# Kernel optimization log

Hardware: AMD Instinct MI355X
Metric: run time of the kernel (lower is better)

## Reference

```python
import jax, jax.numpy as jnp
import numpy as np

B, S, H, DH = 2, 2048, 16, 64
D = H * DH  # 1024
NEG = 1e11

def setup_inputs() -> dict:
    key = jax.random.key(0)
    ks = jax.random.split(key, 4)
    std = 0.02
    return {
        "x": jax.random.normal(ks[0], (B, S, D), dtype=jnp.float32),
        "Wq": jax.random.normal(ks[1], (D, D), dtype=jnp.float32) * std,
        "bq": jnp.zeros((D,), dtype=jnp.float32),
        "Wk": jax.random.normal(ks[2], (D, D), dtype=jnp.float32) * std,
        "bk": jnp.zeros((D,), dtype=jnp.float32),
        "Wv": jax.random.normal(ks[3], (D, D), dtype=jnp.float32) * std,
        "bv": jnp.zeros((D,), dtype=jnp.float32),
    }

def reference(x, Wq, bq, Wk, bk, Wv, bv):
    # QKV projections: [B,S,D]
    q = x @ Wq + bq
    k = x @ Wk + bk
    v = x @ Wv + bv
    # split heads -> [B,H,S,DH]
    def split(t):
        return t.reshape(B, S, H, DH).transpose(0, 2, 1, 3)
    q, k, v = split(q), split(k), split(v)
    # scaled scores [B,H,S,S]
    scores = jnp.einsum("bhqd,bhkd->bhqk", q, k) / jnp.sqrt(jnp.float32(DH))
    # causal mask: query i attends to keys j <= i; original does s*m - (1-m)*1e11
    m = (jnp.arange(S)[:, None] >= jnp.arange(S)[None, :]).astype(scores.dtype)
    scores = scores * m - (1.0 - m) * NEG
    probs = jax.nn.softmax(scores, axis=-1)
    out = jnp.einsum("bhqk,bhkd->bhqd", probs, v)  # [B,H,S,DH]
    return out.transpose(0, 2, 1, 3).reshape(B, S, D)
```

## Files before the change

### kernel.cpp

```cpp
#include <hip/hip_runtime.h>
#include <hip/hip_bf16.h>
#include <stdint.h>

#define B_    2
#define S_    2048
#define H_    16
#define DH_   64
#define D_    1024
#define ND3   3072
#define MTOT  4096
#define L2E   1.4426950408889634f
#define MASKVAL (-3.0e38f)
#define SBIAS   (-14.0f)

typedef __attribute__((ext_vector_type(8))) short bf16x8;
typedef __attribute__((ext_vector_type(4))) short bf16x4;
typedef __attribute__((ext_vector_type(4))) float f32x4;

#if __has_builtin(__builtin_amdgcn_exp2f)
#define EXP2(x) __builtin_amdgcn_exp2f(x)
#else
#define EXP2(x) exp2f(x)
#endif

__device__ inline short f2bs(float f) {
  __hip_bfloat16 h = __float2bfloat16(f);
  return *reinterpret_cast<short*>(&h);
}

__device__ inline void gl_lds16(const void* g, void* l) {
  __builtin_amdgcn_global_load_lds(
      (const __attribute__((address_space(1))) uint32_t*)g,
      (__attribute__((address_space(3))) uint32_t*)l, 16, 0, 0);
}

__global__ __launch_bounds__(256) void prep_kernel(
    const float* __restrict__ X, const float* __restrict__ Wq,
    const float* __restrict__ Wk, const float* __restrict__ Wv,
    short* __restrict__ Xb, short* __restrict__ Wt) {
  __shared__ float t[32][33];
  int bid = blockIdx.x;
  if (bid < 4096) {
    const int i = (bid * 256 + threadIdx.x) * 4;
    float4 v = *reinterpret_cast<const float4*>(X + i);
    bf16x4 o;
    o[0] = f2bs(v.x); o[1] = f2bs(v.y); o[2] = f2bs(v.z); o[3] = f2bs(v.w);
    *reinterpret_cast<bf16x4*>(Xb + i) = o;
  } else {
    bid -= 4096;
    const int z = bid >> 10;
    const int rem = bid & 1023;
    const int n0 = (rem & 31) * 32, k0 = (rem >> 5) * 32;
    const int x = threadIdx.x & 31, y = threadIdx.x >> 5;
    const float* W = z == 0 ? Wq : (z == 1 ? Wk : Wv);
    short* out = Wt + (size_t)z * (D_ * D_);
#pragma unroll
    for (int i = 0; i < 4; ++i)
      t[y + 8 * i][x] = W[(size_t)(k0 + y + 8 * i) * D_ + n0 + x];
    __syncthreads();
#pragma unroll
    for (int i = 0; i < 4; ++i)
      out[(size_t)(n0 + y + 8 * i) * D_ + k0 + x] = f2bs(t[x][y + 8 * i]);
  }
}

__global__ __launch_bounds__(512, 2) void qkv_gemm_kernel(
    const short* __restrict__ Xb, const short* __restrict__ Wt,
    const float* __restrict__ bq, const float* __restrict__ bk,
    const float* __restrict__ bv, short* __restrict__ QKV,
    short* __restrict__ Vt) {
  __shared__ char Lds[114688];
  const int tid = threadIdx.x;
  const int lane = tid & 63;
  const int wid = tid >> 6;
  const int l15 = lane & 15, lg = lane >> 4;
  const int wm = wid >> 2, wn = wid & 3;
  const int bid = blockIdx.x;
  const int wgid = (bid & 7) * 32 + (bid >> 3);
  const int m0 = (wgid >> 4) * 256, n0 = (wgid & 15) * 192;

  const int srow = tid >> 3;
  const int scol = ((tid & 7) ^ (srow & 7)) * 8;
  const short* pa = Xb + (size_t)(m0 + srow) * D_ + scol;
  const short* pb = Wt + (size_t)(n0 + srow) * D_ + scol;
  char* sdst = Lds + (tid & 448) * 16;

  const int abase = wm * 16384;
  int a_off[8][2], b_off[3][2];
#pragma unroll
  for (int mr = 0; mr < 8; ++mr)
#pragma unroll
    for (int ks = 0; ks < 2; ++ks)
      a_off[mr][ks] =
          (mr * 16 + l15) * 128 + ((((ks * 4 + lg)) ^ (l15 & 7)) << 4);
#pragma unroll
  for (int nr = 0; nr < 3; ++nr)
#pragma unroll
    for (int ks = 0; ks < 2; ++ks)
      b_off[nr][ks] = (wn * 48 + nr * 16 + l15) * 128 +
                      ((((ks * 4 + lg)) ^ (l15 & 7)) << 4);

  f32x4 acc[8][3];
#pragma unroll
  for (int i = 0; i < 8; ++i)
#pragma unroll
    for (int j = 0; j < 3; ++j) acc[i][j] = (f32x4){0.f, 0.f, 0.f, 0.f};

#define BARRIER()                                                             \
  __builtin_amdgcn_s_barrier();                                               \
  __builtin_amdgcn_sched_barrier(0)

  gl_lds16(pa, sdst);
  gl_lds16(pa + (size_t)64 * D_, sdst + 8192);
  gl_lds16(pa + (size_t)128 * D_, sdst + 16384);
  gl_lds16(pa + (size_t)192 * D_, sdst + 24576);
  gl_lds16(pb, sdst + 32768);
  gl_lds16(pb + (size_t)64 * D_, sdst + 40960);
  gl_lds16(pb + (size_t)128 * D_, sdst + 49152);
  asm volatile("s_waitcnt vmcnt(0)" ::: "memory");
  BARRIER();

#define TILE(J, DL)                                                           \
  {                                                                           \
    const int j_ = (J);                                                       \
    const bool stg = (j_ + 1 < 16);                                           \
    const int RD = (DL) * 57344;                                              \
    const int WD = (1 - (DL)) * 57344;                                        \
    const short* pa1 = pa + (j_ + 1) * 64;                                    \
    const short* pb1 = pb + (j_ + 1) * 64;                                    \
    bf16x8 af[4], bf0, bf1, bf2;                                              \
       \
    if (stg) {                                                                \
      gl_lds16(pa1, sdst + WD);                                               \
      gl_lds16(pa1 + (size_t)64 * D_, sdst + WD + 8192);                      \
      gl_lds16(pb1, sdst + WD + 32768);                                       \
      gl_lds16(pb1 + (size_t)64 * D_, sdst + WD + 40960);                     \
    }                                                                         \
    bf0 = *reinterpret_cast<const bf16x8*>(Lds + RD + 32768 + b_off[0][0]);   \
    bf1 = *reinterpret_cast<const bf16x8*>(Lds + RD + 32768 + b_off[1][0]);   \
    bf2 = *reinterpret_cast<const bf16x8*>(Lds + RD + 32768 + b_off[2][0]);   \
    _Pragma("unroll") for (int mr = 0; mr < 4; ++mr) af[mr] =                 \
        *reinterpret_cast<const bf16x8*>(Lds + RD + abase + a_off[mr][0]);    \
    BARRIER();                                                                \
    __builtin_amdgcn_s_setprio(1);                                            \
    _Pragma("unroll") for (int mr = 0; mr < 4; ++mr) {                        \
      acc[mr][0] = __builtin_amdgcn_mfma_f32_16x16x32_bf16(af[mr], bf0,       \
                                                           acc[mr][0], 0, 0,  \
                                                           0);                \
      acc[mr][1] = __builtin_amdgcn_mfma_f32_16x16x32_bf16(af[mr], bf1,       \
                                                           acc[mr][1], 0, 0,  \
                                                           0);                \
      acc[mr][2] = __builtin_amdgcn_mfma_f32_16x16x32_bf16(af[mr], bf2,       \
                                                           acc[mr][2], 0, 0,  \
                                                           0);                \
    }                                                                         \
    __builtin_amdgcn_s_setprio(0);                                            \
    BARRIER();                                                                \
                  \
    if (stg) {                                                                \
      gl_lds16(pa1 + (size_t)128 * D_, sdst + WD + 16384);                    \
      gl_lds16(pa1 + (size_t)192 * D_, sdst + WD + 24576);                    \
      gl_lds16(pb1 + (size_t)128 * D_, sdst + WD + 49152);                    \
    }                                                                         \
    _Pragma("unroll") for (int mr = 0; mr < 4; ++mr) af[mr] =                 \
        *reinterpret_cast<const bf16x8*>(Lds + RD + abase +                   \
                                         a_off[mr + 4][0]);                   \
    BARRIER();                                                                \
    __builtin_amdgcn_s_setprio(1);                                            \
    _Pragma("unroll") for (int mr = 0; mr < 4; ++mr) {                        \
      acc[mr + 4][0] = __builtin_amdgcn_mfma_f32_16x16x32_bf16(               \
          af[mr], bf0, acc[mr + 4][0], 0, 0, 0);                              \
      acc[mr + 4][1] = __builtin_amdgcn_mfma_f32_16x16x32_bf16(               \
          af[mr], bf1, acc[mr + 4][1], 0, 0, 0);                              \
      acc[mr + 4][2] = __builtin_amdgcn_mfma_f32_16x16x32_bf16(               \
          af[mr], bf2, acc[mr + 4][2], 0, 0, 0);                              \
    }                                                                         \
    __builtin_amdgcn_s_setprio(0);                                            \
    BARRIER();                                                                \
                           \
    bf0 = *reinterpret_cast<const bf16x8*>(Lds + RD + 32768 + b_off[0][1]);   \
    bf1 = *reinterpret_cast<const bf16x8*>(Lds + RD + 32768 + b_off[1][1]);   \
    bf2 = *reinterpret_cast<const bf16x8*>(Lds + RD + 32768 + b_off[2][1]);   \
    _Pragma("unroll") for (int mr = 0; mr < 4; ++mr) af[mr] =                 \
        *reinterpret_cast<const bf16x8*>(Lds + RD + abase + a_off[mr][1]);    \
    BARRIER();                                                                \
    __builtin_amdgcn_s_setprio(1);                                            \
    _Pragma("unroll") for (int mr = 0; mr < 4; ++mr) {                        \
      acc[mr][0] = __builtin_amdgcn_mfma_f32_16x16x32_bf16(af[mr], bf0,       \
                                                           acc[mr][0], 0, 0,  \
                                                           0);                \
      acc[mr][1] = __builtin_amdgcn_mfma_f32_16x16x32_bf16(af[mr], bf1,       \
                                                           acc[mr][1], 0, 0,  \
                                                           0);                \
      acc[mr][2] = __builtin_amdgcn_mfma_f32_16x16x32_bf16(af[mr], bf2,       \
                                                           acc[mr][2], 0, 0,  \
                                                           0);                \
    }                                                                         \
    __builtin_amdgcn_s_setprio(0);                                            \
    BARRIER();                                                                \
               \
    _Pragma("unroll") for (int mr = 0; mr < 4; ++mr) af[mr] =                 \
        *reinterpret_cast<const bf16x8*>(Lds + RD + abase +                   \
                                         a_off[mr + 4][1]);                   \
    BARRIER();                                                                \
    __builtin_amdgcn_s_setprio(1);                                            \
    _Pragma("unroll") for (int mr = 0; mr < 4; ++mr) {                        \
      acc[mr + 4][0] = __builtin_amdgcn_mfma_f32_16x16x32_bf16(               \
          af[mr], bf0, acc[mr + 4][0], 0, 0, 0);                              \
      acc[mr + 4][1] = __builtin_amdgcn_mfma_f32_16x16x32_bf16(               \
          af[mr], bf1, acc[mr + 4][1], 0, 0, 0);                              \
      acc[mr + 4][2] = __builtin_amdgcn_mfma_f32_16x16x32_bf16(               \
          af[mr], bf2, acc[mr + 4][2], 0, 0, 0);                              \
    }                                                                         \
    __builtin_amdgcn_s_setprio(0);                                            \
    asm volatile("s_waitcnt vmcnt(0)" ::: "memory");                          \
    BARRIER();                                                                \
  }

  for (int jj = 0; jj < 16; jj += 2) {
    TILE(jj, 0);
    TILE(jj + 1, 1);
  }
#undef TILE
#undef BARRIER

  const int wr = wm * 128;
#pragma unroll
  for (int nr = 0; nr < 3; ++nr) {
    const int col = n0 + wn * 48 + nr * 16 + l15;
    if (col < 2 * D_) {
      float bias, qs;
      if (col < D_) { bias = bq[col];      qs = 0.125f * L2E; }
      else          { bias = bk[col - D_]; qs = 1.f; }
#pragma unroll
      for (int mr = 0; mr < 8; ++mr)
#pragma unroll
        for (int r = 0; r < 4; ++r) {
          const int row = m0 + wr + mr * 16 + lg * 4 + r;
          QKV[(size_t)row * ND3 + col] = f2bs((acc[mr][nr][r] + bias) * qs);
        }
    } else {
      const int f = col - 2 * D_;
      const float bias = bv[f];
      const int base0 = (m0 & 2047) + wr;
      short* vout = Vt + ((size_t)((m0 >> 11) * H_ + (f >> 6)) * DH_ +
                          (f & 63)) * S_;
#pragma unroll
      for (int mr = 0; mr < 8; ++mr) {
        bf16x4 pv;
#pragma unroll
        for (int r = 0; r < 4; ++r) pv[r] = f2bs(acc[mr][nr][r] + bias);
        const int ntk = mr & 3;
        const int s_new = base0 + (mr >> 2) * 64 +
                          ((ntk >> 1) * 4 + lg) * 8 + (ntk & 1) * 4;
        *reinterpret_cast<bf16x4*>(vout + s_new) = pv;
      }
    }
  }
}

__global__ __launch_bounds__(256, 4) void attn_kernel(
    const short* __restrict__ QKV, const short* __restrict__ Vtg,
    float* __restrict__ Out) {
  __shared__ short KV[5][4096];
  const int tid = threadIdx.x;
  const int lane = tid & 63, wid = tid >> 6;
  const int l15 = lane & 15, lg = lane >> 4;
  const int bh = blockIdx.x;
  const int qt = (S_ / 64 - 1) - (int)blockIdx.y;
  const int b = bh >> 4, h = bh & 15;
  const int q0 = qt * 64;
  const short* Qg = QKV + (size_t)b * S_ * ND3 + h * DH_;
  const short* Kg = QKV + (size_t)b * S_ * ND3 + D_ + h * DH_;
  const short* Vg = Vtg + (size_t)bh * DH_ * S_;

  const int srow = tid >> 3;
  const int scol = ((tid & 7) ^ (srow & 7)) * 8;
  const char* kbase = (const char*)&KV[0][0];
  char* dst = (char*)kbase + (tid & 192) * 16;
  int ka[2];
#pragma unroll
  for (int ks = 0; ks < 2; ++ks)
    ka[ks] = l15 * 128 + ((((ks * 4 + lg)) ^ (l15 & 7)) << 4);
  const int qrow_g = q0 + wid * 16 + l15;

  bf16x8 qf[2];
#pragma unroll
  for (int ks = 0; ks < 2; ++ks)
    qf[ks] = *reinterpret_cast<const bf16x8*>(Qg + (size_t)qrow_g * ND3 +
                                              ks * 32 + lg * 8);

  const f32x4 cinit = (f32x4){SBIAS, SBIAS, SBIAS, SBIAS};

  f32x4 o[4];
#pragma unroll
  for (int i = 0; i < 4; ++i) o[i] = (f32x4){0.f, 0.f, 0.f, 0.f};
  float lsum = 0.f;

  const short* kp = Kg + (size_t)srow * ND3 + scol;
  const short* vp = Vg + (size_t)srow * S_ + scol;

#define STAGE_AT(KOFF, VOFF)                                                  \
  {                                                                           \
    gl_lds16(kp, dst + (KOFF));                                               \
    gl_lds16(kp + 32 * ND3, dst + (KOFF) + 4096);                             \
    gl_lds16(vp, dst + (VOFF));                                               \
    gl_lds16(vp + 32 * S_, dst + (VOFF) + 4096);                              \
    kp += 64 * ND3;                                                           \
    vp += 64;                                                                 \
  }

  int kr = 8192, kw = 0;
  int vr = 16384, vw = 32768;

  STAGE_AT(0, 16384);
  if (qt >= 1) STAGE_AT(8192, 24576);
  asm volatile("s_waitcnt vmcnt(0)" ::: "memory");
  __builtin_amdgcn_s_barrier();
  __builtin_amdgcn_sched_barrier(0);

  f32x4 sA[4], sB[4];
#pragma unroll
  for (int nt = 0; nt < 4; ++nt)
    sA[nt] = __builtin_amdgcn_mfma_f32_16x16x32_bf16(
        *reinterpret_cast<const bf16x8*>(kbase + ka[0] + nt * 2048), qf[0],
        cinit, 0, 0, 0);
#pragma unroll
  for (int nt = 0; nt < 4; ++nt)
    sA[nt] = __builtin_amdgcn_mfma_f32_16x16x32_bf16(
        *reinterpret_cast<const bf16x8*>(kbase + ka[1] + nt * 2048), qf[1],
        sA[nt], 0, 0, 0);

#define STEP_BODY(T, SC, SN)                                                  \
  {                                                                           \
    const int T_ = (T);                                                       \
    if (T_ + 2 <= qt) STAGE_AT(kw, vw);                                       \
    if (T_ + 1 <= qt) {                                                       \
      _Pragma("unroll") for (int nt = 0; nt < 4; ++nt)                        \
          SN[nt] = __builtin_amdgcn_mfma_f32_16x16x32_bf16(                   \
              *reinterpret_cast<const bf16x8*>(kbase + kr + ka[0] +           \
                                               nt * 2048),                    \
              qf[0], cinit, 0, 0, 0);                                         \
      _Pragma("unroll") for (int nt = 0; nt < 4; ++nt)                        \
          SN[nt] = __builtin_amdgcn_mfma_f32_16x16x32_bf16(                   \
              *reinterpret_cast<const bf16x8*>(kbase + kr + ka[1] +           \
                                               nt * 2048),                    \
              qf[1], SN[nt], 0, 0, 0);                                        \
    }                                                                         \
    if (T_ == qt) {                         \
      const int kv0 = T_ * 64;                                                \
      _Pragma("unroll") for (int nt = 0; nt < 4; ++nt)                        \
        _Pragma("unroll") for (int r = 0; r < 4; ++r)                         \
          if (kv0 + nt * 16 + lg * 4 + r > qrow_g) SC[nt][r] = MASKVAL;       \
    }                                                                         \
    float rowsum = 0.f;                                                       \
    bf16x4 pk[4];                                                             \
    _Pragma("unroll") for (int nt = 0; nt < 4; ++nt) {                        \
      const float p0 = EXP2(SC[nt][0]);                                       \
      const float p1 = EXP2(SC[nt][1]);                                       \
      const float p2 = EXP2(SC[nt][2]);                                       \
      const float p3 = EXP2(SC[nt][3]);                                       \
      rowsum += (p0 + p1) + (p2 + p3);                                        \
      union { uint32_t u[2]; bf16x4 v; } pu;                                  \
      pu.u[0] = __builtin_amdgcn_perm(__float_as_uint(p1),                    \
                                      __float_as_uint(p0), 0x07060302u);      \
      pu.u[1] = __builtin_amdgcn_perm(__float_as_uint(p3),                    \
                                      __float_as_uint(p2), 0x07060302u);      \
      pk[nt] = pu.v;                                                          \
    }                                                                         \
    lsum += rowsum;                                                           \
    _Pragma("unroll") for (int p = 0; p < 2; ++p)                             \
      _Pragma("unroll") for (int ntd = 0; ntd < 4; ++ntd) {                   \
        const bf16x8 vf8 = *reinterpret_cast<const bf16x8*>(                  \
            kbase + vr + ka[p] + ntd * 2048);                                 \
        const bf16x4 vlo = __builtin_shufflevector(vf8, vf8, 0, 1, 2, 3);     \
        const bf16x4 vhi = __builtin_shufflevector(vf8, vf8, 4, 5, 6, 7);     \
        o[ntd] = __builtin_amdgcn_mfma_f32_16x16x16bf16_1k(vlo, pk[2 * p],    \
                                                           o[ntd], 0, 0, 0);  \
        o[ntd] = __builtin_amdgcn_mfma_f32_16x16x16bf16_1k(                   \
            vhi, pk[2 * p + 1], o[ntd], 0, 0, 0);                             \
      }                                                                       \
    if (T_ < qt) {                                                            \
      asm volatile("s_waitcnt vmcnt(0)" ::: "memory");                        \
      __builtin_amdgcn_s_barrier();                                           \
      __builtin_amdgcn_sched_barrier(0);                                      \
    }                                                                         \
    kr ^= 8192; kw ^= 8192;                                                   \
    { const int tv = vr; vr = 73728 - vr - vw; vw = tv; }                     \
  }

  for (int t = 0; t <= qt; t += 2) {
    STEP_BODY(t, sA, sB);
    if (t + 1 <= qt) STEP_BODY(t + 1, sB, sA);
  }
#undef STEP_BODY
#undef STAGE_AT

  float ls = lsum;
  ls += __shfl_xor(ls, 16);
  ls += __shfl_xor(ls, 32);
  const float inv = 1.f / ls;
#pragma unroll
  for (int nt = 0; nt < 4; ++nt) {
    f32x4 v = {o[nt][0] * inv, o[nt][1] * inv, o[nt][2] * inv, o[nt][3] * inv};
    *reinterpret_cast<f32x4*>(
        &Out[((size_t)b * S_ + qrow_g) * D_ + h * DH_ + nt * 16 + lg * 4]) = v;
  }
}

extern "C" void kernel_launch(void* const* d_in, const int* in_sizes, int n_in,
                              void* d_out, int out_size, void* d_ws,
                              size_t ws_size, hipStream_t stream) {
  const float* x  = (const float*)d_in[0];
  const float* Wq = (const float*)d_in[1];
  const float* bq = (const float*)d_in[2];
  const float* Wk = (const float*)d_in[3];
  const float* bk = (const float*)d_in[4];
  const float* Wv = (const float*)d_in[5];
  const float* bv = (const float*)d_in[6];
  float* out = (float*)d_out;

  char* ws = (char*)d_ws;
  short* xb  = (short*)(ws);
  short* Wt  = (short*)(ws + 8388608);
  short* qkv = (short*)(ws + 14680064);
  short* Vt  = (short*)(ws + 39845888);

  prep_kernel<<<dim3(4096 + 3072), dim3(256), 0, stream>>>(x, Wq, Wk, Wv, xb,
                                                           Wt);
  qkv_gemm_kernel<<<dim3(256), dim3(512), 0, stream>>>(xb, Wt, bq, bk, bv,
                                                       qkv, Vt);
  attn_kernel<<<dim3(B_ * H_, S_ / 64), dim3(256), 0, stream>>>(qkv, Vt, out);
}
```

Before: 69.73 us.

## Split attention KV tile across waves and reduce partial outputs in LDS

Reorganizes the attention kernel so each of the four waves handles all 64 query rows against its own 16-key slice of every KV tile, instead of each wave owning 16 query rows against all keys. Partial O accumulators and row sums are then combined across waves through LDS in a tree reduction before the final normalized write. The V-transpose layout in the projection epilogue is simplified to match the new V fragment reads, and the pipeline drops to double buffering with a separate masked final tile. This raises register pressure (16 accumulators plus 8 Q fragments, launch bound lowered to 3 blocks), adds a reduction epilogue with several barriers, and leaves only wave 0 writing the output.

```diff
diff --git a/kernel.cpp b/kernel.cpp
--- a/kernel.cpp
+++ b/kernel.cpp
@@ -242,7 +242,7 @@
     } else {
       const int f = col - 2 * D_;
       const float bias = bv[f];
-      const int base0 = (m0 & 2047) + wr;
+      const int srow_base = (m0 & 2047) + wr + lg * 4;
       short* vout = Vt + ((size_t)((m0 >> 11) * H_ + (f >> 6)) * DH_ +
                           (f & 63)) * S_;
 #pragma unroll
@@ -250,19 +250,16 @@
         bf16x4 pv;
 #pragma unroll
         for (int r = 0; r < 4; ++r) pv[r] = f2bs(acc[mr][nr][r] + bias);
-        const int ntk = mr & 3;
-        const int s_new = base0 + (mr >> 2) * 64 +
-                          ((ntk >> 1) * 4 + lg) * 8 + (ntk & 1) * 4;
-        *reinterpret_cast<bf16x4*>(vout + s_new) = pv;
+        *reinterpret_cast<bf16x4*>(vout + srow_base + mr * 16) = pv;
       }
     }
   }
 }
 
-__global__ __launch_bounds__(256, 4) void attn_kernel(
+__global__ __launch_bounds__(256, 3) void attn_kernel(
     const short* __restrict__ QKV, const short* __restrict__ Vtg,
     float* __restrict__ Out) {
-  __shared__ short KV[5][4096];
+  __shared__ char LB[36864];
   const int tid = threadIdx.x;
   const int lane = tid & 63, wid = tid >> 6;
   const int l15 = lane & 15, lg = lane >> 4;
@@ -276,26 +273,33 @@
 
   const int srow = tid >> 3;
   const int scol = ((tid & 7) ^ (srow & 7)) * 8;
-  const char* kbase = (const char*)&KV[0][0];
-  char* dst = (char*)kbase + (tid & 192) * 16;
+  char* dst = LB + (tid & 192) * 16;
   int ka[2];
 #pragma unroll
   for (int ks = 0; ks < 2; ++ks)
-    ka[ks] = l15 * 128 + ((((ks * 4 + lg)) ^ (l15 & 7)) << 4);
-  const int qrow_g = q0 + wid * 16 + l15;
-
-  bf16x8 qf[2];
-#pragma unroll
-  for (int ks = 0; ks < 2; ++ks)
-    qf[ks] = *reinterpret_cast<const bf16x8*>(Qg + (size_t)qrow_g * ND3 +
-                                              ks * 32 + lg * 8);
+    ka[ks] = (wid * 16 + l15) * 128 + ((((ks * 4 + lg)) ^ (l15 & 7)) << 4);
+  int va[4];
+#pragma unroll
+  for (int ntd = 0; ntd < 4; ++ntd)
+    va[ntd] = (ntd * 16 + l15) * 128 +
+              (((2 * wid + (lg >> 1)) ^ (l15 & 7)) << 4) + ((lg & 1) << 3);
+
+  bf16x8 qf[4][2];
+#pragma unroll
+  for (int qb = 0; qb < 4; ++qb)
+#pragma unroll
+    for (int ks = 0; ks < 2; ++ks)
+      qf[qb][ks] = *reinterpret_cast<const bf16x8*>(
+          Qg + (size_t)(q0 + qb * 16 + l15) * ND3 + ks * 32 + lg * 8);
 
   const f32x4 cinit = (f32x4){SBIAS, SBIAS, SBIAS, SBIAS};
 
-  f32x4 o[4];
-#pragma unroll
-  for (int i = 0; i < 4; ++i) o[i] = (f32x4){0.f, 0.f, 0.f, 0.f};
-  float lsum = 0.f;
+  f32x4 o[4][4];
+#pragma unroll
+  for (int i = 0; i < 4; ++i)
+#pragma unroll
+    for (int j = 0; j < 4; ++j) o[i][j] = (f32x4){0.f, 0.f, 0.f, 0.f};
+  float lsum[4] = {0.f, 0.f, 0.f, 0.f};
 
   const short* kp = Kg + (size_t)srow * ND3 + scol;
   const short* vp = Vg + (size_t)srow * S_ + scol;
@@ -310,102 +314,111 @@
     vp += 64;                                                                 \
   }
 
-  int kr = 8192, kw = 0;
-  int vr = 16384, vw = 32768;
-
-  STAGE_AT(0, 16384);
-  if (qt >= 1) STAGE_AT(8192, 24576);
-  asm volatile("s_waitcnt vmcnt(0)" ::: "memory");
-  __builtin_amdgcn_s_barrier();
-  __builtin_amdgcn_sched_barrier(0);
-
-  f32x4 sA[4], sB[4];
-#pragma unroll
-  for (int nt = 0; nt < 4; ++nt)
-    sA[nt] = __builtin_amdgcn_mfma_f32_16x16x32_bf16(
-        *reinterpret_cast<const bf16x8*>(kbase + ka[0] + nt * 2048), qf[0],
-        cinit, 0, 0, 0);
-#pragma unroll
-  for (int nt = 0; nt < 4; ++nt)
-    sA[nt] = __builtin_amdgcn_mfma_f32_16x16x32_bf16(
-        *reinterpret_cast<const bf16x8*>(kbase + ka[1] + nt * 2048), qf[1],
-        sA[nt], 0, 0, 0);
-
-#define STEP_BODY(T, SC, SN)                                                  \
+#define COMPUTE(SP, MASKED, KV0)                                              \
   {                                                                           \
-    const int T_ = (T);                                                       \
-    if (T_ + 2 <= qt) STAGE_AT(kw, vw);                                       \
-    if (T_ + 1 <= qt) {                                                       \
-      _Pragma("unroll") for (int nt = 0; nt < 4; ++nt)                        \
-          SN[nt] = __builtin_amdgcn_mfma_f32_16x16x32_bf16(                   \
-              *reinterpret_cast<const bf16x8*>(kbase + kr + ka[0] +           \
-                                               nt * 2048),                    \
-              qf[0], cinit, 0, 0, 0);                                         \
-      _Pragma("unroll") for (int nt = 0; nt < 4; ++nt)                        \
-          SN[nt] = __builtin_amdgcn_mfma_f32_16x16x32_bf16(                   \
-              *reinterpret_cast<const bf16x8*>(kbase + kr + ka[1] +           \
-                                               nt * 2048),                    \
-              qf[1], SN[nt], 0, 0, 0);                                        \
-    }                                                                         \
-    if (T_ == qt) {                         \
-      const int kv0 = T_ * 64;                                                \
-      _Pragma("unroll") for (int nt = 0; nt < 4; ++nt)                        \
+    const char* kb = LB + (SP) * 8192;                                        \
+    const char* vb = LB + 16384 + (SP) * 8192;                                \
+    const bf16x8 kf0 = *reinterpret_cast<const bf16x8*>(kb + ka[0]);          \
+    const bf16x8 kf1 = *reinterpret_cast<const bf16x8*>(kb + ka[1]);          \
+    f32x4 s[4];                                                               \
+    _Pragma("unroll") for (int qb = 0; qb < 4; ++qb)                          \
+        s[qb] = __builtin_amdgcn_mfma_f32_16x16x32_bf16(kf0, qf[qb][0],       \
+                                                        cinit, 0, 0, 0);      \
+    _Pragma("unroll") for (int qb = 0; qb < 4; ++qb)                          \
+        s[qb] = __builtin_amdgcn_mfma_f32_16x16x32_bf16(kf1, qf[qb][1],       \
+                                                        s[qb], 0, 0, 0);      \
+    if (MASKED) {           \
+      const int kvg = (KV0) + wid * 16 + lg * 4;                              \
+      _Pragma("unroll") for (int qb = 0; qb < 4; ++qb)                        \
         _Pragma("unroll") for (int r = 0; r < 4; ++r)                         \
-          if (kv0 + nt * 16 + lg * 4 + r > qrow_g) SC[nt][r] = MASKVAL;       \
-    }                                                                         \
-    float rowsum = 0.f;                                                       \
+          if (kvg + r > q0 + qb * 16 + l15) s[qb][r] = MASKVAL;               \
+    }                                                                         \
     bf16x4 pk[4];                                                             \
-    _Pragma("unroll") for (int nt = 0; nt < 4; ++nt) {                        \
-      const float p0 = EXP2(SC[nt][0]);                                       \
-      const float p1 = EXP2(SC[nt][1]);                                       \
-      const float p2 = EXP2(SC[nt][2]);                                       \
-      const float p3 = EXP2(SC[nt][3]);                                       \
-      rowsum += (p0 + p1) + (p2 + p3);                                        \
+    _Pragma("unroll") for (int qb = 0; qb < 4; ++qb) {                        \
+      const float p0 = EXP2(s[qb][0]);                                        \
+      const float p1 = EXP2(s[qb][1]);                                        \
+      const float p2 = EXP2(s[qb][2]);                                        \
+      const float p3 = EXP2(s[qb][3]);                                        \
+      lsum[qb] += (p0 + p1) + (p2 + p3);                                      \
       union { uint32_t u[2]; bf16x4 v; } pu;                                  \
       pu.u[0] = __builtin_amdgcn_perm(__float_as_uint(p1),                    \
                                       __float_as_uint(p0), 0x07060302u);      \
       pu.u[1] = __builtin_amdgcn_perm(__float_as_uint(p3),                    \
                                       __float_as_uint(p2), 0x07060302u);      \
-      pk[nt] = pu.v;                                                          \
-    }                                                                         \
-    lsum += rowsum;                                                           \
-    _Pragma("unroll") for (int p = 0; p < 2; ++p)                             \
-      _Pragma("unroll") for (int ntd = 0; ntd < 4; ++ntd) {                   \
-        const bf16x8 vf8 = *reinterpret_cast<const bf16x8*>(                  \
-            kbase + vr + ka[p] + ntd * 2048);                                 \
-        const bf16x4 vlo = __builtin_shufflevector(vf8, vf8, 0, 1, 2, 3);     \
-        const bf16x4 vhi = __builtin_shufflevector(vf8, vf8, 4, 5, 6, 7);     \
-        o[ntd] = __builtin_amdgcn_mfma_f32_16x16x16bf16_1k(vlo, pk[2 * p],    \
-                                                           o[ntd], 0, 0, 0);  \
-        o[ntd] = __builtin_amdgcn_mfma_f32_16x16x16bf16_1k(                   \
-            vhi, pk[2 * p + 1], o[ntd], 0, 0, 0);                             \
-      }                                                                       \
-    if (T_ < qt) {                                                            \
-      asm volatile("s_waitcnt vmcnt(0)" ::: "memory");                        \
-      __builtin_amdgcn_s_barrier();                                           \
-      __builtin_amdgcn_sched_barrier(0);                                      \
-    }                                                                         \
-    kr ^= 8192; kw ^= 8192;                                                   \
-    { const int tv = vr; vr = 73728 - vr - vw; vw = tv; }                     \
-  }
-
-  for (int t = 0; t <= qt; t += 2) {
-    STEP_BODY(t, sA, sB);
-    if (t + 1 <= qt) STEP_BODY(t + 1, sB, sA);
-  }
-#undef STEP_BODY
+      pk[qb] = pu.v;                                                          \
+    }                                                                         \
+    _Pragma("unroll") for (int ntd = 0; ntd < 4; ++ntd) {                     \
+      const bf16x4 vf = *reinterpret_cast<const bf16x4*>(vb + va[ntd]);       \
+      _Pragma("unroll") for (int qb = 0; qb < 4; ++qb)                        \
+          o[ntd][qb] = __builtin_amdgcn_mfma_f32_16x16x16bf16_1k(             \
+              vf, pk[qb], o[ntd][qb], 0, 0, 0);                               \
+    }                                                                         \
+  }
+
+  STAGE_AT(0, 16384);
+  asm volatile("s_waitcnt vmcnt(0)" ::: "memory");
+  __builtin_amdgcn_s_barrier();
+  __builtin_amdgcn_sched_barrier(0);
+
+  int sp = 0;
+  for (int t = 0; t < qt; ++t) {
+    STAGE_AT((sp ^ 1) * 8192, 16384 + (sp ^ 1) * 8192);
+    COMPUTE(sp, false, 0);
+    asm volatile("s_waitcnt vmcnt(0)" ::: "memory");
+    __builtin_amdgcn_s_barrier();
+    __builtin_amdgcn_sched_barrier(0);
+    sp ^= 1;
+  }
+  COMPUTE(sp, true, qt * 64);
+#undef COMPUTE
 #undef STAGE_AT
 
-  float ls = lsum;
-  ls += __shfl_xor(ls, 16);
-  ls += __shfl_xor(ls, 32);
-  const float inv = 1.f / ls;
-#pragma unroll
-  for (int nt = 0; nt < 4; ++nt) {
-    f32x4 v = {o[nt][0] * inv, o[nt][1] * inv, o[nt][2] * inv, o[nt][3] * inv};
-    *reinterpret_cast<f32x4*>(
-        &Out[((size_t)b * S_ + qrow_g) * D_ + h * DH_ + nt * 16 + lg * 4]) = v;
-  }
+  __builtin_amdgcn_s_barrier();
+  float* lsLDS = reinterpret_cast<float*>(LB + 32768);
+#pragma unroll
+  for (int qb = 0; qb < 4; ++qb) lsLDS[wid * 256 + qb * 64 + lane] = lsum[qb];
+#define OWRITE(RG)                                                            \
+  _Pragma("unroll") for (int ntd = 0; ntd < 4; ++ntd)                         \
+    _Pragma("unroll") for (int qb = 0; qb < 4; ++qb)                          \
+        *reinterpret_cast<f32x4*>(LB + (RG) + ((ntd * 4 + qb) * 64 + lane) *  \
+                                                  16) = o[ntd][qb];
+#define OADD(RG)                                                              \
+  _Pragma("unroll") for (int ntd = 0; ntd < 4; ++ntd)                         \
+    _Pragma("unroll") for (int qb = 0; qb < 4; ++qb)                          \
+        o[ntd][qb] += *reinterpret_cast<const f32x4*>(                        \
+            LB + (RG) + ((ntd * 4 + qb) * 64 + lane) * 16);
+  if (wid == 1) { OWRITE(0); }
+  if (wid == 3) { OWRITE(16384); }
+  __builtin_amdgcn_s_barrier();
+  if (wid == 0) { OADD(0); }
+  if (wid == 2) { OADD(16384); }
+  __builtin_amdgcn_s_barrier();
+  if (wid == 2) { OWRITE(0); }
+  __builtin_amdgcn_s_barrier();
+  if (wid == 0) {
+    OADD(0);
+#pragma unroll
+    for (int qb = 0; qb < 4; ++qb) {
+      float ls = lsLDS[0 * 256 + qb * 64 + lane] +
+                 lsLDS[1 * 256 + qb * 64 + lane] +
+                 lsLDS[2 * 256 + qb * 64 + lane] +
+                 lsLDS[3 * 256 + qb * 64 + lane];
+      ls += __shfl_xor(ls, 16);
+      ls += __shfl_xor(ls, 32);
+      const float inv = 1.f / ls;
+      const int qrow = q0 + qb * 16 + l15;
+#pragma unroll
+      for (int ntd = 0; ntd < 4; ++ntd) {
+        f32x4 v = {o[ntd][qb][0] * inv, o[ntd][qb][1] * inv,
+                   o[ntd][qb][2] * inv, o[ntd][qb][3] * inv};
+        *reinterpret_cast<f32x4*>(
+            &Out[((size_t)b * S_ + qrow) * D_ + h * DH_ + ntd * 16 +
+                 lg * 4]) = v;
+      }
+    }
+  }
+#undef OWRITE
+#undef OADD
 }
 
 extern "C" void kernel_launch(void* const* d_in, const int* in_sizes, int n_in,
```

Measured after the change: 74.01 us. 1.06x slower.
